# Kernel optimization log

Measured on AMD Instinct MI355X. Metric: run time of the kernel, lower is better.

The kernel has to match this reference:

```python
import jax, jax.numpy as jnp
import numpy as np

LEN_M = 131328   # (data_dim+1) * d_h = 513 * 256
D_H = 256
N_MC = 64
DATA_DIM_P1 = 513
N = 4096


def setup_inputs() -> dict:
    key = jax.random.key(0)
    k1, k2, k3, k4 = jax.random.split(key, 4)
    params = jax.random.normal(k1, (2 * LEN_M,), dtype=jnp.float32)
    W1 = jax.random.normal(k2, (D_H + 1,), dtype=jnp.float32)
    x = jax.random.normal(k3, (N, DATA_DIM_P1), dtype=jnp.float32)
    eps = jax.random.normal(k4, (N_MC,), dtype=jnp.float32)
    return {"params": params, "W1": W1, "x": x, "eps": eps}


def reference(params, W1, x, eps):
    # split variational params into means and (relu'd) variances
    m_w0 = params[:LEN_M]                                  # [len_m]
    v_w0 = jax.nn.relu(params[LEN_M:]) + 1e-6              # [len_m]
    # reparameterized MC sampling; NOTE: torch code draws ONE scalar eps per
    # MC sample (randn(m_w0[0].shape) is scalar), shared across all weights.
    samps_w0 = m_w0[:, None] + eps[None, :] * jnp.sqrt(v_w0)[:, None]  # [len_m, M]
    W0 = samps_w0.reshape(DATA_DIM_P1, D_H, N_MC)          # [d+1, h, M]
    # fused batched GEMM replacing the d_h * num_MC_samps tiny matmuls
    x_w0 = jnp.einsum('nd,dhm->nhm', x, W0)                # [N, h, M]
    z = jax.nn.relu(x_w0)
    ones = jnp.ones((x.shape[0], 1, N_MC), dtype=x.dtype)
    z = jnp.concatenate([ones, z], axis=1)                 # [N, h+1, M]
    pred_samps = jnp.einsum('nhm,h->nm', z, W1)            # [N, M]
    return pred_samps, m_w0, v_w0
```

## Files before the change

### kernel.cpp

```cpp
#include <hip/hip_runtime.h>
#include <hip/hip_bf16.h>
#include <math.h>

#define LEN_M   131328
#define D_P1    513
#define NROW    4096
#define PRED_ELEMS (NROW * 64)

typedef __attribute__((ext_vector_type(8))) short short8;
typedef __attribute__((ext_vector_type(4))) float floatx4;
typedef __attribute__((ext_vector_type(2))) float v2f;

__device__ __forceinline__ void gl_lds16(const void* g, void* l)
{
    __builtin_amdgcn_global_load_lds(
        (const __attribute__((address_space(1))) unsigned int*)g,
        (__attribute__((address_space(3))) unsigned int*)l, 16, 0, 0);
}

__device__ __forceinline__ unsigned short bf16b(float f)
{
    __hip_bfloat16 h = __float2bfloat16(f);
    return *(unsigned short*)&h;
}

__global__ __launch_bounds__(256) void prep_kernel(
    const float* __restrict__ params, float* __restrict__ out,
    __hip_bfloat16* __restrict__ wcbt)
{
    __shared__ unsigned short T[64][65];
    const int bid = blockIdx.x;
    const int t   = threadIdx.x;

    if (bid < 513) {
        int i = bid * 256 + t;
        float m = params[i];
        float v = fmaxf(params[LEN_M + i], 0.0f) + 1e-6f;
        out[PRED_ELEMS + i]         = m;
        out[PRED_ELEMS + LEN_M + i] = v;
        return;
    }
    if (bid < 769) {
        int i = (bid - 513) * 1024 + t * 4;
        float4 z = {0.f, 0.f, 0.f, 0.f};
        *(float4*)(out + i) = z;
        return;
    }

    const int b2 = bid - 769;
    const int k0 = (b2 & 7) * 64;
    const int c0 = (b2 >> 3) * 64;
    const int hh = t & 63, kb = t >> 6;
    const bool spart = (c0 >= 256);
    const int hbase = c0 & 255;
    const float* src = params + (spart ? LEN_M : 0);

    #pragma unroll 4
    for (int p = 0; p < 16; ++p) {
        int kk = p * 4 + kb;
        float v = src[(k0 + kk) * 256 + hbase + hh];
        if (spart) v = sqrtf(fmaxf(v, 0.0f) + 1e-6f);
        T[kk][hh] = bf16b(v);
    }
    __syncthreads();

    const int cc = t >> 2, kq = t & 3;
    short8 lo, hi;
    #pragma unroll
    for (int j = 0; j < 8; ++j) lo[j] = (short)T[kq * 16 + j][cc];
    #pragma unroll
    for (int j = 0; j < 8; ++j) hi[j] = (short)T[kq * 16 + 8 + j][cc];

    const int cR = c0 + cc;
    const int g1 = (k0 >> 3) + 2 * kq;
    const int g2 = g1 + 1;
    const int d1 = (g1 >> 3) * 4096 + cR * 8 + ((g1 & 7) ^ (cR & 7));
    const int d2 = (g2 >> 3) * 4096 + cR * 8 + ((g2 & 7) ^ (cR & 7));
    short* wb = (short*)wcbt;
    *(short8*)(wb + d1 * 8) = lo;
    *(short8*)(wb + d2 * 8) = hi;
}

__global__ __launch_bounds__(512) void main_kernel(
    const __hip_bfloat16* __restrict__ wcbt, const float* __restrict__ params,
    const float* __restrict__ x, const float* __restrict__ W1,
    const float* __restrict__ eps, float* __restrict__ out)
{
    extern __shared__ char smem[];
    char*  Ap = smem + 65536;
    float* Cl = (float*)smem;

    const int t = threadIdx.x;
    const int w = t >> 6, lane = t & 63;
    const int lane15 = lane & 15, quad = lane >> 4;
    const int ax7 = lane15 & 7;
    const int half = blockIdx.x & 1;
    const int bm   = (blockIdx.x >> 1) * 16;
    const int hoff8 = half * 1024;

    const char* wbase = (const char*)wcbt;

    #pragma unroll
    for (int i = 0; i < 4; ++i) {
        int j = i * 512 + t;
        int src = hoff8 + j + (j & 1024);
        gl_lds16(wbase + src * 16, smem + j * 16);
    }

    {
        const int r = t >> 5, seg = t & 31;
        const float* xrow = x + (bm + r) * D_P1 + seg * 16;
        #pragma unroll
        for (int c2 = 0; c2 < 2; ++c2) {
            int g  = seg * 2 + c2;
            int cs = (g & ~7) | ((g & 7) ^ (r & 7));
            short8 pk;
            #pragma unroll
            for (int j = 0; j < 8; ++j) pk[j] = (short)bf16b(xrow[c2 * 8 + j]);
            *(short8*)(Ap + r * 1024 + cs * 16) = pk;
        }
    }

    const float e = eps[lane];
    float xl[4];
    #pragma unroll
    for (int i = 0; i < 4; ++i)
        xl[i] = x[(bm + quad * 4 + i) * D_P1 + 512];
    int   lc[2];  float wl[2];
    #pragma unroll
    for (int s = 0; s < 2; ++s) {
        lc[s] = w * 32 + s * 16 + lane15;
        int gc = half * 128 + lc[s] + (lc[s] & 128);
        wl[s] = (gc < 256) ? params[131072 + gc]
                           : sqrtf(fmaxf(params[LEN_M + 131072 + (gc - 256)], 0.0f) + 1e-6f);
    }
    const int cb0 = lc[0] * 128, cb1 = lc[1] * 128;

    floatx4 acc0 = {0.f,0.f,0.f,0.f}, acc1 = acc0;

    __syncthreads();

    for (int kc = 0; kc < 8; ++kc) {
        if (kc < 7) {
            char* nbuf = smem + ((kc + 1) & 1) * 32768;
            #pragma unroll
            for (int i = 0; i < 4; ++i) {
                int j = i * 512 + t;
                int src = (kc + 1) * 4096 + hoff8 + j + (j & 1024);
                gl_lds16(wbase + src * 16, nbuf + j * 16);
            }
        }
        const char* Bb = smem + (kc & 1) * 32768;
        const char* Ab = Ap + lane15 * 1024 + kc * 128;
        #pragma unroll
        for (int kk = 0; kk < 2; ++kk) {
            const int off = ((kk * 4 + quad) ^ ax7) * 16;
            short8 a  = *(const short8*)(Ab + off);
            short8 b0 = *(const short8*)(Bb + cb0 + off);
            short8 b1 = *(const short8*)(Bb + cb1 + off);
            acc0 = __builtin_amdgcn_mfma_f32_16x16x32_bf16(a, b0, acc0, 0, 0, 0);
            acc1 = __builtin_amdgcn_mfma_f32_16x16x32_bf16(a, b1, acc1, 0, 0, 0);
        }
        __syncthreads();
    }

    {
        floatx4 accs[2] = {acc0, acc1};
        #pragma unroll
        for (int s = 0; s < 2; ++s) {
            float4 o;
            o.x = accs[s][0] + xl[0] * wl[s];
            o.y = accs[s][1] + xl[1] * wl[s];
            o.z = accs[s][2] + xl[2] * wl[s];
            o.w = accs[s][3] + xl[3] * wl[s];
            *(float4*)&Cl[lc[s] * 20 + quad * 4] = o;
        }
    }
    __syncthreads();

    const int rq = w * 2;
    v2f accp = {0.f, 0.f};
    const v2f e2 = {e, e}, z2 = {0.f, 0.f};

    #pragma unroll 8
    for (int hh = 0; hh < 128; ++hh) {
        const float w1h = W1[1 + half * 128 + hh];
        const v2f w2 = {w1h, w1h};
        const v2f av = *(const v2f*)&Cl[hh * 20 + rq];
        const v2f bv = *(const v2f*)&Cl[(128 + hh) * 20 + rq];
        v2f tt = __builtin_elementwise_max(__builtin_elementwise_fma(e2, bv, av), z2);
        accp = __builtin_elementwise_fma(tt, w2, accp);
    }
    if (half == 0) {
        const float b0 = W1[0];
        accp.x += b0; accp.y += b0;
    }

    float* op = out + (bm + rq) * 64 + lane;
    unsafeAtomicAdd(op,      accp.x);
    unsafeAtomicAdd(op + 64, accp.y);
}

extern "C" void kernel_launch(void* const* d_in, const int* in_sizes, int n_in,
                              void* d_out, int out_size, void* d_ws, size_t ws_size,
                              hipStream_t stream)
{
    const float* params = (const float*)d_in[0];
    const float* W1     = (const float*)d_in[1];
    const float* x      = (const float*)d_in[2];
    const float* eps    = (const float*)d_in[3];
    float* out = (float*)d_out;
    __hip_bfloat16* wcbt = (__hip_bfloat16*)d_ws;

    static bool attr_set = false;
    if (!attr_set) {
        hipFuncSetAttribute((const void*)main_kernel,
                            hipFuncAttributeMaxDynamicSharedMemorySize, 81920);
        attr_set = true;
    }

    prep_kernel<<<833, 256, 0, stream>>>(params, out, wcbt);
    main_kernel<<<512, 512, 81920, stream>>>(wcbt, params, x, W1, eps, out);
}
```

Measured before the change: 84.53 us.

## Retile main kernel to 32 rows by 64 hidden columns per block

The main kernel's block tiling changes from 16 rows by 128 hidden units (two halves) to 32 rows by 64 hidden units (four quarters). Each weight tile staged in LDS is now reused across twice as many x rows, which halves the per-block weight traffic and the LDS buffer size (64KB instead of 80KB). The cost is that x is loaded twice as often and there are four atomic partial sums per output instead of two. The epilogue reduction is restructured to process four rows per wave.

```diff
diff --git a/kernel.cpp b/kernel.cpp
--- a/kernel.cpp
+++ b/kernel.cpp
@@ -87,54 +87,65 @@
     const float* __restrict__ eps, float* __restrict__ out)
 {
     extern __shared__ char smem[];
-    char*  Ap = smem + 65536;
+    char*  Ap = smem + 32768;
     float* Cl = (float*)smem;
 
     const int t = threadIdx.x;
     const int w = t >> 6, lane = t & 63;
     const int lane15 = lane & 15, quad = lane >> 4;
     const int ax7 = lane15 & 7;
-    const int half = blockIdx.x & 1;
-    const int bm   = (blockIdx.x >> 1) * 16;
-    const int hoff8 = half * 1024;
+    const int q  = blockIdx.x & 3;
+    const int bm = (blockIdx.x >> 2) * 32;
 
     const char* wbase = (const char*)wcbt;
 
-    #pragma unroll
-    for (int i = 0; i < 4; ++i) {
-        int j = i * 512 + t;
-        int src = hoff8 + j + (j & 1024);
-        gl_lds16(wbase + src * 16, smem + j * 16);
-    }
-
+    int bsrc_c0, bsrc_c1;
     {
-        const int r = t >> 5, seg = t & 31;
-        const float* xrow = x + (bm + r) * D_P1 + seg * 16;
+        int j0 = t, j1 = 512 + t;
+        int lc0 = j0 >> 3, g0 = j0 & 7;
+        int lc1 = j1 >> 3, g1 = j1 & 7;
+        int cg0 = q * 64 + (lc0 & 63) + ((lc0 >> 6) * 256);
+        int cg1 = q * 64 + (lc1 & 63) + ((lc1 >> 6) * 256);
+        bsrc_c0 = cg0 * 8 + g0;
+        bsrc_c1 = cg1 * 8 + g1;
+    }
+
+    gl_lds16(wbase + bsrc_c0 * 16, smem + t * 16);
+    gl_lds16(wbase + bsrc_c1 * 16, smem + (512 + t) * 16);
+
+    {
+        const int r = t >> 4, seg0 = t & 15;
+        const float* xrow = x + (bm + r) * D_P1;
         #pragma unroll
-        for (int c2 = 0; c2 < 2; ++c2) {
-            int g  = seg * 2 + c2;
-            int cs = (g & ~7) | ((g & 7) ^ (r & 7));
-            short8 pk;
+        for (int ss = 0; ss < 2; ++ss) {
+            const int seg = seg0 + ss * 16;
             #pragma unroll
-            for (int j = 0; j < 8; ++j) pk[j] = (short)bf16b(xrow[c2 * 8 + j]);
-            *(short8*)(Ap + r * 1024 + cs * 16) = pk;
+            for (int c2 = 0; c2 < 2; ++c2) {
+                int g  = seg * 2 + c2;
+                int cs = (g & ~7) | ((g & 7) ^ (r & 7));
+                short8 pk;
+                #pragma unroll
+                for (int j = 0; j < 8; ++j)
+                    pk[j] = (short)bf16b(xrow[seg * 16 + c2 * 8 + j]);
+                *(short8*)(Ap + r * 1024 + cs * 16) = pk;
+            }
         }
     }
 
     const float e = eps[lane];
+    const int rh = w & 1;
+    const int ct = w >> 1;
     float xl[4];
     #pragma unroll
     for (int i = 0; i < 4; ++i)
-        xl[i] = x[(bm + quad * 4 + i) * D_P1 + 512];
-    int   lc[2];  float wl[2];
-    #pragma unroll
-    for (int s = 0; s < 2; ++s) {
-        lc[s] = w * 32 + s * 16 + lane15;
-        int gc = half * 128 + lc[s] + (lc[s] & 128);
-        wl[s] = (gc < 256) ? params[131072 + gc]
-                           : sqrtf(fmaxf(params[LEN_M + 131072 + (gc - 256)], 0.0f) + 1e-6f);
-    }
-    const int cb0 = lc[0] * 128, cb1 = lc[1] * 128;
+        xl[i] = x[(bm + rh * 16 + quad * 4 + i) * D_P1 + 512];
+    const int gc0 = q * 64 + ct * 16 + lane15;
+    const float wl0 = params[131072 + gc0];
+    const float wl1 = sqrtf(fmaxf(params[LEN_M + 131072 + gc0], 0.0f) + 1e-6f);
+
+    const int cb0 = (ct * 16 + lane15) * 128;
+    const int cb1 = cb0 + 64 * 128;
+    const char* Abase = Ap + (rh * 16 + lane15) * 1024;
 
     floatx4 acc0 = {0.f,0.f,0.f,0.f}, acc1 = acc0;
 
@@ -142,16 +153,13 @@
 
     for (int kc = 0; kc < 8; ++kc) {
         if (kc < 7) {
-            char* nbuf = smem + ((kc + 1) & 1) * 32768;
-            #pragma unroll
-            for (int i = 0; i < 4; ++i) {
-                int j = i * 512 + t;
-                int src = (kc + 1) * 4096 + hoff8 + j + (j & 1024);
-                gl_lds16(wbase + src * 16, nbuf + j * 16);
-            }
+            char* nbuf = smem + ((kc + 1) & 1) * 16384;
+            const char* src = wbase + (kc + 1) * 65536;
+            gl_lds16(src + bsrc_c0 * 16, nbuf + t * 16);
+            gl_lds16(src + bsrc_c1 * 16, nbuf + (512 + t) * 16);
         }
-        const char* Bb = smem + (kc & 1) * 32768;
-        const char* Ab = Ap + lane15 * 1024 + kc * 128;
+        const char* Bb = smem + (kc & 1) * 16384;
+        const char* Ab = Abase + kc * 128;
         #pragma unroll
         for (int kk = 0; kk < 2; ++kk) {
             const int off = ((kk * 4 + quad) ^ ax7) * 16;
@@ -165,40 +173,44 @@
     }
 
     {
-        floatx4 accs[2] = {acc0, acc1};
-        #pragma unroll
-        for (int s = 0; s < 2; ++s) {
-            float4 o;
-            o.x = accs[s][0] + xl[0] * wl[s];
-            o.y = accs[s][1] + xl[1] * wl[s];
-            o.z = accs[s][2] + xl[2] * wl[s];
-            o.w = accs[s][3] + xl[3] * wl[s];
-            *(float4*)&Cl[lc[s] * 20 + quad * 4] = o;
-        }
+        const int r0 = rh * 16 + quad * 4;
+        float4 o0, o1;
+        o0.x = acc0[0] + xl[0] * wl0;  o1.x = acc1[0] + xl[0] * wl1;
+        o0.y = acc0[1] + xl[1] * wl0;  o1.y = acc1[1] + xl[1] * wl1;
+        o0.z = acc0[2] + xl[2] * wl0;  o1.z = acc1[2] + xl[2] * wl1;
+        o0.w = acc0[3] + xl[3] * wl0;  o1.w = acc1[3] + xl[3] * wl1;
+        *(float4*)&Cl[(ct * 16 + lane15) * 36 + r0]      = o0;
+        *(float4*)&Cl[(64 + ct * 16 + lane15) * 36 + r0] = o1;
     }
     __syncthreads();
 
-    const int rq = w * 2;
-    v2f accp = {0.f, 0.f};
+    const int rw = w * 4;
+    v2f accp0 = {0.f, 0.f}, accp1 = {0.f, 0.f};
     const v2f e2 = {e, e}, z2 = {0.f, 0.f};
 
     #pragma unroll 8
-    for (int hh = 0; hh < 128; ++hh) {
-        const float w1h = W1[1 + half * 128 + hh];
+    for (int hh = 0; hh < 64; ++hh) {
+        const float w1h = W1[1 + q * 64 + hh];
         const v2f w2 = {w1h, w1h};
-        const v2f av = *(const v2f*)&Cl[hh * 20 + rq];
-        const v2f bv = *(const v2f*)&Cl[(128 + hh) * 20 + rq];
-        v2f tt = __builtin_elementwise_max(__builtin_elementwise_fma(e2, bv, av), z2);
-        accp = __builtin_elementwise_fma(tt, w2, accp);
-    }
-    if (half == 0) {
+        const float4 av = *(const float4*)&Cl[hh * 36 + rw];
+        const float4 bv = *(const float4*)&Cl[(64 + hh) * 36 + rw];
+        v2f a01 = {av.x, av.y}, a23 = {av.z, av.w};
+        v2f b01 = {bv.x, bv.y}, b23 = {bv.z, bv.w};
+        v2f t01 = __builtin_elementwise_max(__builtin_elementwise_fma(e2, b01, a01), z2);
+        v2f t23 = __builtin_elementwise_max(__builtin_elementwise_fma(e2, b23, a23), z2);
+        accp0 = __builtin_elementwise_fma(t01, w2, accp0);
+        accp1 = __builtin_elementwise_fma(t23, w2, accp1);
+    }
+    if (q == 0) {
         const float b0 = W1[0];
-        accp.x += b0; accp.y += b0;
-    }
-
-    float* op = out + (bm + rq) * 64 + lane;
-    unsafeAtomicAdd(op,      accp.x);
-    unsafeAtomicAdd(op + 64, accp.y);
+        accp0.x += b0; accp0.y += b0; accp1.x += b0; accp1.y += b0;
+    }
+
+    float* op = out + (bm + rw) * 64 + lane;
+    unsafeAtomicAdd(op,       accp0.x);
+    unsafeAtomicAdd(op + 64,  accp0.y);
+    unsafeAtomicAdd(op + 128, accp1.x);
+    unsafeAtomicAdd(op + 192, accp1.y);
 }
 
 extern "C" void kernel_launch(void* const* d_in, const int* in_sizes, int n_in,
@@ -215,10 +227,10 @@
     static bool attr_set = false;
     if (!attr_set) {
         hipFuncSetAttribute((const void*)main_kernel,
-                            hipFuncAttributeMaxDynamicSharedMemorySize, 81920);
+                            hipFuncAttributeMaxDynamicSharedMemorySize, 65536);
         attr_set = true;
     }
 
     prep_kernel<<<833, 256, 0, stream>>>(params, out, wcbt);
-    main_kernel<<<512, 512, 81920, stream>>>(wcbt, params, x, W1, eps, out);
-}
+    main_kernel<<<512, 512, 65536, stream>>>(wcbt, params, x, W1, eps, out);
+}
```

New measurement: 82.11 us, median of 2. -2.9%, faster.
